# Kernel tuning notes

Measured on AMD Instinct MI355X. Metric: run time of the kernel, lower is better.

## Reference

```python
import jax, jax.numpy as jnp
import numpy as np

C = 128
NUM_GROUPS = 32  # min(32, 128 // 4)
EPS = 1e-6


def group_norm(x, gamma, beta):
    N, Cc, H, W = x.shape
    xg = x.reshape(N, NUM_GROUPS, -1)
    mean = xg.mean(axis=-1, keepdims=True)
    var = ((xg - mean) ** 2).mean(axis=-1, keepdims=True)
    xn = ((xg - mean) * jax.lax.rsqrt(var + EPS)).reshape(N, Cc, H, W)
    return xn * gamma[None, :, None, None] + beta[None, :, None, None]


def conv1x1(x, w, b):
    # w: [C_out, C_in], b: [C_out]; 1x1 conv == channel matmul
    return jnp.einsum('nchw,oc->nohw', x, w) + b[None, :, None, None]


def setup_inputs() -> dict:
    key = jax.random.key(0)
    ks = jax.random.split(key, 11)
    s = 1.0 / np.sqrt(C)
    return {
        'x': jax.random.normal(ks[0], (4, C, 64, 64), dtype=jnp.float32),
        'gamma': jnp.ones((C,), jnp.float32),
        'beta': jnp.zeros((C,), jnp.float32),
        'wq': jax.random.normal(ks[1], (C, C), jnp.float32) * s,
        'bq': jnp.zeros((C,), jnp.float32),
        'wk': jax.random.normal(ks[2], (C, C), jnp.float32) * s,
        'bk': jnp.zeros((C,), jnp.float32),
        'wv': jax.random.normal(ks[3], (C, C), jnp.float32) * s,
        'bv': jnp.zeros((C,), jnp.float32),
        'wo': jax.random.normal(ks[4], (C, C), jnp.float32) * s,
        'bo': jnp.zeros((C,), jnp.float32),
    }


def reference(x, gamma, beta, wq, bq, wk, bk, wv, bv, wo, bo):
    N, Cc, H, W = x.shape
    L = H * W
    xn = group_norm(x, gamma, beta)
    q = conv1x1(xn, wq, bq).reshape(N, Cc, L)  # [N,C,L]
    k = conv1x1(xn, wk, bk).reshape(N, Cc, L)
    v = conv1x1(xn, wv, bv).reshape(N, Cc, L)
    scale = 1.0 / jnp.sqrt(jnp.asarray(Cc, x.dtype))
    scores = jnp.einsum('ncl,ncm->nlm', q, k) * scale  # [N,L,L]
    weights = jax.nn.softmax(scores, axis=-1)
    attn = jnp.einsum('nlm,ncm->ncl', weights, v).reshape(N, Cc, H, W)
    return x + conv1x1(attn, wo, bo)
```

## Files before the change

kernel.cpp:

```cpp
#include <hip/hip_runtime.h>
#include <hip/hip_bf16.h>


#define N_B 4
#define C_D 128
#define L_D 4096
#define SPLIT 4
#define KVB 128
#define FSTEPS ((L_D/SPLIT)/KVB)
#define QSCALE (0.08838834764831845f * 1.4426950408889634f)
#define FIXM 16.0f

using f32x4  = __attribute__((ext_vector_type(4))) float;
using f32x16 = __attribute__((ext_vector_type(16))) float;
using bf16x8 = __attribute__((ext_vector_type(8))) short;

static __device__ __forceinline__ unsigned short f2bf(float f){
  return (unsigned short)((__builtin_bit_cast(unsigned int, f) + 0x8000u) >> 16);
}
static __device__ __forceinline__ float bf2f(unsigned short u){
  unsigned int x = ((unsigned int)u) << 16;
  return __builtin_bit_cast(float, x);
}
static __device__ __forceinline__ unsigned int pk2(float a, float b){
  unsigned int ua = __builtin_bit_cast(unsigned int, a) + 0x8000u;
  unsigned int ub = __builtin_bit_cast(unsigned int, b) + 0x8000u;
  return __builtin_amdgcn_perm(ub, ua, 0x07060302u);
}
static __device__ __forceinline__ float exp2a(float x){
  float r; asm("v_exp_f32 %0, %1" : "=v"(r) : "v"(x)); return r;
}
static __device__ __forceinline__ void gll16(const void* g, void* l){
  __builtin_amdgcn_global_load_lds(
      (const __attribute__((address_space(1))) unsigned int*)g,
      (__attribute__((address_space(3))) unsigned int*)l, 16, 0, 0);
}

__global__ __launch_bounds__(256) void gnw_k(
    const float* __restrict__ x, float* __restrict__ stats,
    const float* __restrict__ wq, const float* __restrict__ wk,
    const float* __restrict__ wv, const float* __restrict__ wo,
    unsigned short* __restrict__ wbf)
{
  int b = blockIdx.x, t = threadIdx.x;
  if (b >= 128){
    int b2 = b - 128;
    int mat = b2 >> 4;
    const float* src = (mat == 0) ? wq : (mat == 1) ? wk : (mat == 2) ? wv : wo;
    int off = (b2 & 15) * 1024 + t * 4;
    float4 v = *(const float4*)(src + off);
    *(uint2*)(wbf + mat*16384 + off) = make_uint2(pk2(v.x, v.y), pk2(v.z, v.w));
    return;
  }
  const float4* p = (const float4*)(x + (size_t)b * (4 * L_D));
  float s = 0.f, ss = 0.f;
#pragma unroll
  for (int i = 0; i < 16; ++i){
    float4 v = p[t + i*256];
    s  += v.x + v.y + v.z + v.w;
    ss += v.x*v.x + v.y*v.y + v.z*v.z + v.w*v.w;
  }
#pragma unroll
  for (int off = 32; off > 0; off >>= 1){
    s  += __shfl_down(s, off);
    ss += __shfl_down(ss, off);
  }
  __shared__ float rs4[4], rss4[4];
  if ((t & 63) == 0){ rs4[t>>6] = s; rss4[t>>6] = ss; }
  __syncthreads();
  if (t == 0){
    s  = rs4[0]+rs4[1]+rs4[2]+rs4[3];
    ss = rss4[0]+rss4[1]+rss4[2]+rss4[3];
    float mean = s * (1.f/16384.f);
    float var  = ss * (1.f/16384.f) - mean*mean;
    if (var < 0.f) var = 0.f;
    stats[2*b]   = mean;
    stats[2*b+1] = rsqrtf(var + 1e-6f);
  }
}

__global__ __launch_bounds__(256) void qkv_k(
    const float* __restrict__ x, const float* __restrict__ stats,
    const float* __restrict__ gamma, const float* __restrict__ beta,
    const unsigned short* __restrict__ wbf,
    const float* __restrict__ bq, const float* __restrict__ bk,
    const float* __restrict__ bv,
    unsigned short* __restrict__ q_ws, unsigned short* __restrict__ k_ws,
    unsigned short* __restrict__ v_ws)
{
  __shared__ unsigned short xnT[64][136];
  __shared__ unsigned short qbuf[64][136];

  int t = threadIdx.x, b = blockIdx.x;
  int wi = b >> 8;
  int bt = b & 255;
  int n = bt >> 6, l0 = (bt & 63) * 64;

  {
    int l = t & 63, cq = t >> 6;
#pragma unroll
    for (int it = 0; it < 8; ++it){
      int c0 = cq*4 + it*16;
      int g  = c0 >> 2;
      float mean = stats[(n*32+g)*2];
      float rstd = stats[(n*32+g)*2+1];
      float vv[4];
#pragma unroll
      for (int jj = 0; jj < 4; ++jj){
        int c = c0 + jj;
        float sc = rstd * gamma[c];
        float bs = beta[c] - mean * sc;
        vv[jj] = x[(size_t)(n*C_D + c)*L_D + l0 + l]*sc + bs;
      }
      *(unsigned int*)&xnT[l][c0]   = pk2(vv[0], vv[1]);
      *(unsigned int*)&xnT[l][c0+2] = pk2(vv[2], vv[3]);
    }
  }
  __syncthreads();

  int w = t >> 6, lane = t & 63, u = lane >> 4, l15 = lane & 15;
  int wc = w >> 1, wl = w & 1;
  const unsigned short* W = wbf + wi*16384;
  const float* Bv = (wi == 0) ? bq : (wi == 1) ? bk : bv;

  f32x4 zz = {0.f,0.f,0.f,0.f};
  f32x4 acc[4][2];
#pragma unroll
  for (int ct = 0; ct < 4; ++ct)
#pragma unroll
    for (int lt = 0; lt < 2; ++lt) acc[ct][lt] = zz;

#pragma unroll
  for (int kst = 0; kst < 4; ++kst){
    bf16x8 bfrag[2];
#pragma unroll
    for (int lt = 0; lt < 2; ++lt)
      bfrag[lt] = *(const bf16x8*)&xnT[32*wl + 16*lt + l15][kst*32 + 8*u];
#pragma unroll
    for (int ct = 0; ct < 4; ++ct){
      bf16x8 af = *(const bf16x8*)(W + (size_t)(64*wc + 16*ct + l15)*C_D + kst*32 + 8*u);
#pragma unroll
      for (int lt = 0; lt < 2; ++lt)
        acc[ct][lt] = __builtin_amdgcn_mfma_f32_16x16x32_bf16(af, bfrag[lt], acc[ct][lt], 0, 0, 0);
    }
  }

  if (wi < 2){
    float qs = (wi == 0) ? QSCALE : 1.0f;
#pragma unroll
    for (int ct = 0; ct < 4; ++ct){
      float bias[4];
#pragma unroll
      for (int r = 0; r < 4; ++r) bias[r] = Bv[64*wc + 16*ct + 4*u + r];
#pragma unroll
      for (int lt = 0; lt < 2; ++lt){
        float v0 = (acc[ct][lt][0] + bias[0]) * qs;
        float v1 = (acc[ct][lt][1] + bias[1]) * qs;
        float v2 = (acc[ct][lt][2] + bias[2]) * qs;
        float v3 = (acc[ct][lt][3] + bias[3]) * qs;
        int row = 32*wl + 16*lt + l15;
        int col = 64*wc + 16*ct + 4*u;
        *(unsigned int*)&qbuf[row][col]   = pk2(v0, v1);
        *(unsigned int*)&qbuf[row][col+2] = pk2(v2, v3);
      }
    }
    __syncthreads();
    {
      int l = t >> 2, ch = t & 3;
      unsigned short* dst = ((wi == 0) ? q_ws : k_ws) + (size_t)(n*L_D + l0 + l)*C_D + ch*32;
#pragma unroll
      for (int i = 0; i < 4; ++i)
        *(uint4*)(dst + i*8) = *(const uint4*)&qbuf[l][ch*32 + i*8];
    }
  } else {
    int p16 = (l15 & 3) | ((l15 & 4) << 1) | ((l15 & 8) >> 1);
#pragma unroll
    for (int ct = 0; ct < 4; ++ct){
      float bias[4];
#pragma unroll
      for (int r = 0; r < 4; ++r) bias[r] = Bv[64*wc + 16*ct + 4*u + r];
#pragma unroll
      for (int lt = 0; lt < 2; ++lt)
#pragma unroll
        for (int r = 0; r < 4; ++r){
          int co = 64*wc + 16*ct + 4*u + r;
          v_ws[(size_t)(n*C_D + co)*L_D + l0 + 32*wl + 16*lt + p16] =
              f2bf(acc[ct][lt][r] + bias[r]);
        }
    }
  }
}

__global__ __launch_bounds__(512, 2) void flash_split_k(
    const unsigned short* __restrict__ q_ws, const unsigned short* __restrict__ k_ws,
    const unsigned short* __restrict__ v_ws,
    unsigned short* __restrict__ po_ws, float* __restrict__ md_ws)
{
  __shared__ __align__(16) char shmem[131072];

  int t = threadIdx.x;
  int phys = blockIdx.x;
  int xcd = phys & 7, j = phys >> 3;
  int pair = xcd*8 + (j & 7);
  int s = j >> 3;
  int n = pair >> 4, lt256 = pair & 15;
  int l0 = lt256 * 256;
  int m_base = s * (L_D / SPLIT);
  int w = t >> 6, lane = t & 63, hi = lane >> 5, l31 = lane & 31;
  int lr = lane >> 4, ls = lane & 15;

  bf16x8 qf[8];
  {
    const unsigned short* qrow = q_ws + ((size_t)(n*L_D + l0 + 32*w + l31))*C_D;
#pragma unroll
    for (int kst = 0; kst < 8; ++kst)
      qf[kst] = *(const bf16x8*)(qrow + 16*kst + 8*hi);
  }

  f32x16 zz16;
#pragma unroll
  for (int i = 0; i < 16; ++i) zz16[i] = 0.f;
  f32x16 accO[4];
#pragma unroll
  for (int ct = 0; ct < 4; ++ct) accO[ct] = zz16;
  float rsum = 0.f;

  const unsigned short* kg[4];
  const unsigned short* vg[4];
  int ldof[4];
#pragma unroll
  for (int i = 0; i < 4; ++i){
    int row = 16*w + 4*i + lr;
    int ub = (ls << 4) ^ ((row & 15) << 4);
    kg[i] = k_ws + ((size_t)(n*L_D + m_base + row))*C_D + (ub >> 1);
    vg[i] = v_ws + ((size_t)(n*C_D + row))*L_D + m_base + (ub >> 1);
    ldof[i] = (16*w + 4*i)*256;
  }

  {
#pragma unroll
    for (int i = 0; i < 4; ++i){
      gll16(kg[i], shmem + ldof[i]);
      gll16(vg[i], shmem + 65536 + ldof[i]);
    }
  }
  __syncthreads();

#pragma unroll 2
  for (int step = 0; step < FSTEPS; ++step){
    int cur = step & 1, nxt = cur ^ 1;
    char* kB = shmem + (cur << 15);
    char* vB = shmem + 65536 + (cur << 15);

    if (step + 1 < FSTEPS){
      char* kN = shmem + (nxt << 15);
      char* vN = shmem + 65536 + (nxt << 15);
#pragma unroll
      for (int i = 0; i < 4; ++i){
        gll16(kg[i] + (size_t)(step+1)*KVB*C_D, kN + ldof[i]);
        gll16(vg[i] + (step+1)*KVB,             vN + ldof[i]);
      }
    }

    f32x16 accS[4];
#pragma unroll
    for (int mt = 0; mt < 4; ++mt) accS[mt] = zz16;
    __builtin_amdgcn_s_setprio(1);
#pragma unroll
    for (int mt = 0; mt < 4; ++mt){
      int row = 32*mt + l31;
      bf16x8 afr[8];
#pragma unroll
      for (int kst = 0; kst < 8; ++kst)
        afr[kst] = *(const bf16x8*)(kB + row*256 + ((32*kst + 16*hi) ^ ((row & 15) << 4)));
#pragma unroll
      for (int kst = 0; kst < 8; ++kst)
        accS[mt] = __builtin_amdgcn_mfma_f32_32x32x16_bf16(afr[kst], qf[kst], accS[mt], 0, 0, 0);
    }
    __builtin_amdgcn_s_setprio(0);

    union { unsigned int u[8]; bf16x8 h[2]; } Wm[4];
#pragma unroll
    for (int mt = 0; mt < 4; ++mt){
      float p[16];
#pragma unroll
      for (int r = 0; r < 16; ++r){ p[r] = exp2a(accS[mt][r] - FIXM); rsum += p[r]; }
#pragma unroll
      for (int wd = 0; wd < 8; ++wd) Wm[mt].u[wd] = pk2(p[2*wd], p[2*wd+1]);
    }

    __builtin_amdgcn_s_setprio(1);
#pragma unroll
    for (int sl = 0; sl < 8; ++sl){
      bf16x8 pf = Wm[sl >> 1].h[sl & 1];
      bf16x8 vfr[4];
#pragma unroll
      for (int ct = 0; ct < 4; ++ct){
        int vr = 32*ct + l31;
        vfr[ct] = *(const bf16x8*)(vB + vr*256 + ((32*sl + 16*hi) ^ ((vr & 15) << 4)));
      }
#pragma unroll
      for (int ct = 0; ct < 4; ++ct)
        accO[ct] = __builtin_amdgcn_mfma_f32_32x32x16_bf16(vfr[ct], pf, accO[ct], 0, 0, 0);
    }
    __builtin_amdgcn_s_setprio(0);
    __syncthreads();
  }

  rsum += __shfl_xor(rsum, 32);

  char* tB = shmem;
  {
    int lloc = 32*w + l31;
    int tsw = (lloc & 15) << 4;
    char* tr = tB + (size_t)lloc*256;
#pragma unroll
    for (int ct = 0; ct < 4; ++ct)
#pragma unroll
      for (int q = 0; q < 4; ++q){
        int cb2 = 64*ct + 16*q + 8*hi;
        *(unsigned int*)(tr + ((cb2    ) ^ tsw)) = pk2(accO[ct][4*q+0], accO[ct][4*q+1]);
        *(unsigned int*)(tr + ((cb2 + 4) ^ tsw)) = pk2(accO[ct][4*q+2], accO[ct][4*q+3]);
      }
  }
  __syncthreads();
  {
    int row2 = t >> 1, hf2 = t & 1;
    int tile = row2 >> 7, lrow = row2 & 127;
    size_t pb = ((size_t)((n*32 + 2*lt256 + tile)*SPLIT + s)) * (size_t)(128*128);
    unsigned short* dst = po_ws + pb + (size_t)lrow*128 + hf2*64;
    const char* srcr = tB + row2*256;
    int sw2 = (row2 & 15) << 4;
#pragma unroll
    for (int i = 0; i < 8; ++i)
      *(uint4*)(dst + 8*i) = *(const uint4*)(srcr + ((hf2*128 + 16*i) ^ sw2));
  }
  if (lane < 32){
    int lg = 32*w + lane;
    int tile2 = lg >> 7, lrow2 = lg & 127;
    size_t mb2 = ((size_t)((n*32 + 2*lt256 + tile2)*SPLIT + s)) * 128;
    md_ws[mb2 + lrow2] = rsum;
  }
}

__global__ __launch_bounds__(256) void combine_k(
    const unsigned short* __restrict__ po_ws, const float* __restrict__ md_ws,
    const float* __restrict__ x, const unsigned short* __restrict__ wo_bf,
    const float* __restrict__ bo, float* __restrict__ out)
{
  __shared__ __align__(16) char aB[16384];

  int t = threadIdx.x, b = blockIdx.x;
  int xcd = b & 7, j = b >> 3;
  int pair = xcd*8 + (j & 7);
  int quarter = j >> 3;
  int n = pair >> 4, lt256 = pair & 15;
  int lt64 = lt256*4 + quarter;
  int f = lt64 >> 1, loff = (lt64 & 1)*64, l0 = lt64*64;
  size_t pbase = ((size_t)((n*32 + f)*SPLIT)) * (size_t)(128*128);
  size_t mbase = ((size_t)((n*32 + f)*SPLIT)) * 128;

  {
    int l = t >> 2, q = t & 3;
    float Dg = 0.f;
#pragma unroll
    for (int s2 = 0; s2 < SPLIT; ++s2)
      Dg += md_ws[mbase + s2*128 + loff + l];
    float inv = 1.0f / Dg;

    float a[32];
#pragma unroll
    for (int i = 0; i < 32; ++i) a[i] = 0.f;
#pragma unroll
    for (int s2 = 0; s2 < SPLIT; ++s2){
      const uint4* p = (const uint4*)(po_ws + pbase + (size_t)s2*(128*128)
                                      + (size_t)(loff + l)*128 + q*32);
#pragma unroll
      for (int i = 0; i < 4; ++i){
        uint4 uv = p[i];
        unsigned int uu[4] = {uv.x, uv.y, uv.z, uv.w};
#pragma unroll
        for (int j2 = 0; j2 < 4; ++j2){
          a[8*i + 2*j2]     += bf2f((unsigned short)(uu[j2] & 0xffffu));
          a[8*i + 2*j2 + 1] += bf2f((unsigned short)(uu[j2] >> 16));
        }
      }
    }
    char* ar = aB + l*256;
    int asw = (l & 7) << 4;
#pragma unroll
    for (int i = 0; i < 16; ++i){
      int cb = q*64 + 4*i;
      *(unsigned int*)(ar + (cb ^ asw)) = pk2(a[2*i]*inv, a[2*i+1]*inv);
    }
  }
  __syncthreads();

  int w = t >> 6, lane = t & 63, hi = lane >> 5, l31 = lane & 31;
  int lh = w >> 1, ch = w & 1;
  f32x16 acc[2];
#pragma unroll
  for (int ci = 0; ci < 2; ++ci)
#pragma unroll
    for (int i = 0; i < 16; ++i) acc[ci][i] = 0.f;

#pragma unroll
  for (int kst = 0; kst < 8; ++kst){
    int row = 32*lh + l31;
    bf16x8 bfg = *(const bf16x8*)(aB + row*256 + ((32*kst + 16*hi) ^ ((row & 7) << 4)));
#pragma unroll
    for (int ci = 0; ci < 2; ++ci){
      bf16x8 af = *(const bf16x8*)(wo_bf + (size_t)(64*ch + 32*ci + l31)*C_D + 16*kst + 8*hi);
      acc[ci] = __builtin_amdgcn_mfma_f32_32x32x16_bf16(af, bfg, acc[ci], 0, 0, 0);
    }
  }
#pragma unroll
  for (int ci = 0; ci < 2; ++ci)
#pragma unroll
    for (int r = 0; r < 16; ++r){
      int o = 64*ch + 32*ci + (r & 3) + 8*(r >> 2) + 4*hi;
      size_t idx = (size_t)(n*C_D + o)*L_D + l0 + 32*lh + l31;
      out[idx] = x[idx] + bo[o] + acc[ci][r];
    }
}

extern "C" void kernel_launch(void* const* d_in, const int* in_sizes, int n_in,
                              void* d_out, int out_size, void* d_ws, size_t ws_size,
                              hipStream_t stream) {
  const float* x     = (const float*)d_in[0];
  const float* gamma = (const float*)d_in[1];
  const float* beta  = (const float*)d_in[2];
  const float* wq    = (const float*)d_in[3];
  const float* bq    = (const float*)d_in[4];
  const float* wk    = (const float*)d_in[5];
  const float* bk    = (const float*)d_in[6];
  const float* wv    = (const float*)d_in[7];
  const float* bv    = (const float*)d_in[8];
  const float* wo    = (const float*)d_in[9];
  const float* bo    = (const float*)d_in[10];
  float* out = (float*)d_out;

  char* ws = (char*)d_ws;
  float* stats          = (float*)ws;
  unsigned short* q_ws  = (unsigned short*)(ws + 4096);
  unsigned short* k_ws  = q_ws + (size_t)N_B * L_D * C_D;
  unsigned short* v_ws  = k_ws + (size_t)N_B * L_D * C_D;
  unsigned short* po_ws = v_ws + (size_t)N_B * L_D * C_D;
  float* md_ws          = (float*)(po_ws + (size_t)N_B * 32 * SPLIT * 128 * 128);
  unsigned short* wbf   = (unsigned short*)(md_ws + (size_t)N_B * 32 * SPLIT * 128);

  gnw_k<<<192, 256, 0, stream>>>(x, stats, wq, wk, wv, wo, wbf);
  qkv_k<<<768, 256, 0, stream>>>(x, stats, gamma, beta, wbf, bq, bk, bv,
                                 q_ws, k_ws, v_ws);
  flash_split_k<<<256, 512, 0, stream>>>(q_ws, k_ws, v_ws, po_ws, md_ws);
  combine_k<<<256, 256, 0, stream>>>(po_ws, md_ws, x, wbf + 3*16384, bo, out);
}
```

Baseline: 73.77 us.

## Fuse output projection into flash kernel, drop KV split, precompute normalized x

The flash attention kernel no longer splits the key/value range across blocks. Each block covers 64 query rows over the full sequence, and its 8 waves split the key tiles and reduce partial outputs through shared memory. The output projection and residual add now happen inside the flash kernel, which removes the combine kernel and the partial-output workspace traffic. The group-norm kernel writes normalized bf16 activations directly, and the QKV kernel loops over all three weight matrices per block. In exchange there are fewer blocks in flight, each block runs longer over the full sequence, and the cross-wave reduction adds shared-memory traffic.

```diff
diff --git a/kernel.cpp b/kernel.cpp
--- a/kernel.cpp
+++ b/kernel.cpp
@@ -5,9 +5,6 @@
 #define N_B 4
 #define C_D 128
 #define L_D 4096
-#define SPLIT 4
-#define KVB 128
-#define FSTEPS ((L_D/SPLIT)/KVB)
 #define QSCALE (0.08838834764831845f * 1.4426950408889634f)
 #define FIXM 16.0f
 
@@ -37,10 +34,11 @@
 }
 
 __global__ __launch_bounds__(256) void gnw_k(
-    const float* __restrict__ x, float* __restrict__ stats,
+    const float* __restrict__ x,
+    const float* __restrict__ gamma, const float* __restrict__ beta,
     const float* __restrict__ wq, const float* __restrict__ wk,
     const float* __restrict__ wv, const float* __restrict__ wo,
-    unsigned short* __restrict__ wbf)
+    unsigned short* __restrict__ wbf, unsigned short* __restrict__ xn)
 {
   int b = blockIdx.x, t = threadIdx.x;
   if (b >= 128){
@@ -53,10 +51,12 @@
     return;
   }
   const float4* p = (const float4*)(x + (size_t)b * (4 * L_D));
+  float4 vbuf[16];
   float s = 0.f, ss = 0.f;
 #pragma unroll
   for (int i = 0; i < 16; ++i){
     float4 v = p[t + i*256];
+    vbuf[i] = v;
     s  += v.x + v.y + v.z + v.w;
     ss += v.x*v.x + v.y*v.y + v.z*v.z + v.w*v.w;
   }
@@ -68,20 +68,35 @@
   __shared__ float rs4[4], rss4[4];
   if ((t & 63) == 0){ rs4[t>>6] = s; rss4[t>>6] = ss; }
   __syncthreads();
-  if (t == 0){
-    s  = rs4[0]+rs4[1]+rs4[2]+rs4[3];
-    ss = rss4[0]+rss4[1]+rss4[2]+rss4[3];
-    float mean = s * (1.f/16384.f);
-    float var  = ss * (1.f/16384.f) - mean*mean;
-    if (var < 0.f) var = 0.f;
-    stats[2*b]   = mean;
-    stats[2*b+1] = rsqrtf(var + 1e-6f);
+  s  = rs4[0]+rs4[1]+rs4[2]+rs4[3];
+  ss = rss4[0]+rss4[1]+rss4[2]+rss4[3];
+  float mean = s * (1.f/16384.f);
+  float var  = ss * (1.f/16384.f) - mean*mean;
+  if (var < 0.f) var = 0.f;
+  float rstd = rsqrtf(var + 1e-6f);
+
+  int cb = (b & 31) * 4;
+  float scv[4], bsv[4];
+#pragma unroll
+  for (int ch = 0; ch < 4; ++ch){
+    scv[ch] = rstd * gamma[cb + ch];
+    bsv[ch] = beta[cb + ch] - mean * scv[ch];
+  }
+  unsigned short* xo = xn + (size_t)b * (4 * L_D);
+#pragma unroll
+  for (int i = 0; i < 16; ++i){
+    int j  = t + i*256;
+    int ch = j >> 10;
+    float4 v = vbuf[i];
+    float sc = scv[ch], bs = bsv[ch];
+    float v0 = v.x*sc + bs, v1 = v.y*sc + bs;
+    float v2 = v.z*sc + bs, v3 = v.w*sc + bs;
+    *(uint2*)(xo + (size_t)j*4) = make_uint2(pk2(v0, v1), pk2(v2, v3));
   }
 }
 
 __global__ __launch_bounds__(256) void qkv_k(
-    const float* __restrict__ x, const float* __restrict__ stats,
-    const float* __restrict__ gamma, const float* __restrict__ beta,
+    const unsigned short* __restrict__ xn,
     const unsigned short* __restrict__ wbf,
     const float* __restrict__ bq, const float* __restrict__ bk,
     const float* __restrict__ bv,
@@ -92,126 +107,125 @@
   __shared__ unsigned short qbuf[64][136];
 
   int t = threadIdx.x, b = blockIdx.x;
-  int wi = b >> 8;
-  int bt = b & 255;
-  int n = bt >> 6, l0 = (bt & 63) * 64;
+  int n = b >> 6, l0 = (b & 63) * 64;
 
   {
     int l = t & 63, cq = t >> 6;
+    const unsigned short* xr = xn + ((size_t)n*C_D)*L_D + l0 + l;
 #pragma unroll
     for (int it = 0; it < 8; ++it){
       int c0 = cq*4 + it*16;
-      int g  = c0 >> 2;
-      float mean = stats[(n*32+g)*2];
-      float rstd = stats[(n*32+g)*2+1];
-      float vv[4];
-#pragma unroll
-      for (int jj = 0; jj < 4; ++jj){
-        int c = c0 + jj;
-        float sc = rstd * gamma[c];
-        float bs = beta[c] - mean * sc;
-        vv[jj] = x[(size_t)(n*C_D + c)*L_D + l0 + l]*sc + bs;
-      }
-      *(unsigned int*)&xnT[l][c0]   = pk2(vv[0], vv[1]);
-      *(unsigned int*)&xnT[l][c0+2] = pk2(vv[2], vv[3]);
+      unsigned int u0 = xr[(size_t)(c0+0)*L_D];
+      unsigned int u1 = xr[(size_t)(c0+1)*L_D];
+      unsigned int u2 = xr[(size_t)(c0+2)*L_D];
+      unsigned int u3 = xr[(size_t)(c0+3)*L_D];
+      *(unsigned int*)&xnT[l][c0]   = u0 | (u1 << 16);
+      *(unsigned int*)&xnT[l][c0+2] = u2 | (u3 << 16);
     }
   }
   __syncthreads();
 
   int w = t >> 6, lane = t & 63, u = lane >> 4, l15 = lane & 15;
   int wc = w >> 1, wl = w & 1;
-  const unsigned short* W = wbf + wi*16384;
-  const float* Bv = (wi == 0) ? bq : (wi == 1) ? bk : bv;
-
   f32x4 zz = {0.f,0.f,0.f,0.f};
-  f32x4 acc[4][2];
-#pragma unroll
-  for (int ct = 0; ct < 4; ++ct)
-#pragma unroll
-    for (int lt = 0; lt < 2; ++lt) acc[ct][lt] = zz;
-
-#pragma unroll
-  for (int kst = 0; kst < 4; ++kst){
-    bf16x8 bfrag[2];
-#pragma unroll
-    for (int lt = 0; lt < 2; ++lt)
-      bfrag[lt] = *(const bf16x8*)&xnT[32*wl + 16*lt + l15][kst*32 + 8*u];
-#pragma unroll
-    for (int ct = 0; ct < 4; ++ct){
-      bf16x8 af = *(const bf16x8*)(W + (size_t)(64*wc + 16*ct + l15)*C_D + kst*32 + 8*u);
+
+  for (int wi = 0; wi < 3; ++wi){
+    const unsigned short* W = wbf + wi*16384;
+    const float* Bv = (wi == 0) ? bq : (wi == 1) ? bk : bv;
+
+    f32x4 acc[4][2];
+#pragma unroll
+    for (int ct = 0; ct < 4; ++ct)
+#pragma unroll
+      for (int lt = 0; lt < 2; ++lt) acc[ct][lt] = zz;
+
+#pragma unroll
+    for (int kst = 0; kst < 4; ++kst){
+      bf16x8 bfrag[2];
 #pragma unroll
       for (int lt = 0; lt < 2; ++lt)
-        acc[ct][lt] = __builtin_amdgcn_mfma_f32_16x16x32_bf16(af, bfrag[lt], acc[ct][lt], 0, 0, 0);
-    }
-  }
-
-  if (wi < 2){
-    float qs = (wi == 0) ? QSCALE : 1.0f;
-#pragma unroll
-    for (int ct = 0; ct < 4; ++ct){
-      float bias[4];
-#pragma unroll
-      for (int r = 0; r < 4; ++r) bias[r] = Bv[64*wc + 16*ct + 4*u + r];
-#pragma unroll
-      for (int lt = 0; lt < 2; ++lt){
-        float v0 = (acc[ct][lt][0] + bias[0]) * qs;
-        float v1 = (acc[ct][lt][1] + bias[1]) * qs;
-        float v2 = (acc[ct][lt][2] + bias[2]) * qs;
-        float v3 = (acc[ct][lt][3] + bias[3]) * qs;
-        int row = 32*wl + 16*lt + l15;
-        int col = 64*wc + 16*ct + 4*u;
-        *(unsigned int*)&qbuf[row][col]   = pk2(v0, v1);
-        *(unsigned int*)&qbuf[row][col+2] = pk2(v2, v3);
-      }
-    }
-    __syncthreads();
-    {
-      int l = t >> 2, ch = t & 3;
-      unsigned short* dst = ((wi == 0) ? q_ws : k_ws) + (size_t)(n*L_D + l0 + l)*C_D + ch*32;
-#pragma unroll
-      for (int i = 0; i < 4; ++i)
-        *(uint4*)(dst + i*8) = *(const uint4*)&qbuf[l][ch*32 + i*8];
-    }
-  } else {
-    int p16 = (l15 & 3) | ((l15 & 4) << 1) | ((l15 & 8) >> 1);
-#pragma unroll
-    for (int ct = 0; ct < 4; ++ct){
-      float bias[4];
-#pragma unroll
-      for (int r = 0; r < 4; ++r) bias[r] = Bv[64*wc + 16*ct + 4*u + r];
-#pragma unroll
-      for (int lt = 0; lt < 2; ++lt)
-#pragma unroll
-        for (int r = 0; r < 4; ++r){
-          int co = 64*wc + 16*ct + 4*u + r;
-          v_ws[(size_t)(n*C_D + co)*L_D + l0 + 32*wl + 16*lt + p16] =
-              f2bf(acc[ct][lt][r] + bias[r]);
+        bfrag[lt] = *(const bf16x8*)&xnT[32*wl + 16*lt + l15][kst*32 + 8*u];
+#pragma unroll
+      for (int ct = 0; ct < 4; ++ct){
+        bf16x8 af = *(const bf16x8*)(W + (size_t)(64*wc + 16*ct + l15)*C_D + kst*32 + 8*u);
+#pragma unroll
+        for (int lt = 0; lt < 2; ++lt)
+          acc[ct][lt] = __builtin_amdgcn_mfma_f32_16x16x32_bf16(af, bfrag[lt], acc[ct][lt], 0, 0, 0);
+      }
+    }
+
+    if (wi < 2){
+      float qs = (wi == 0) ? QSCALE : 1.0f;
+      __syncthreads();
+#pragma unroll
+      for (int ct = 0; ct < 4; ++ct){
+        float bias[4];
+#pragma unroll
+        for (int r = 0; r < 4; ++r) bias[r] = Bv[64*wc + 16*ct + 4*u + r];
+#pragma unroll
+        for (int lt = 0; lt < 2; ++lt){
+          float v0 = (acc[ct][lt][0] + bias[0]) * qs;
+          float v1 = (acc[ct][lt][1] + bias[1]) * qs;
+          float v2 = (acc[ct][lt][2] + bias[2]) * qs;
+          float v3 = (acc[ct][lt][3] + bias[3]) * qs;
+          int row = 32*wl + 16*lt + l15;
+          int col = 64*wc + 16*ct + 4*u;
+          *(unsigned int*)&qbuf[row][col]   = pk2(v0, v1);
+          *(unsigned int*)&qbuf[row][col+2] = pk2(v2, v3);
         }
-    }
-  }
-}
-
-__global__ __launch_bounds__(512, 2) void flash_split_k(
+      }
+      __syncthreads();
+      {
+        int l = t >> 2, ch = t & 3;
+        unsigned short* dst = ((wi == 0) ? q_ws : k_ws) + (size_t)(n*L_D + l0 + l)*C_D + ch*32;
+#pragma unroll
+        for (int i = 0; i < 4; ++i)
+          *(uint4*)(dst + i*8) = *(const uint4*)&qbuf[l][ch*32 + i*8];
+      }
+    } else {
+      int p16 = (l15 & 3) | ((l15 & 4) << 1) | ((l15 & 8) >> 1);
+#pragma unroll
+      for (int ct = 0; ct < 4; ++ct){
+        float bias[4];
+#pragma unroll
+        for (int r = 0; r < 4; ++r) bias[r] = Bv[64*wc + 16*ct + 4*u + r];
+#pragma unroll
+        for (int lt = 0; lt < 2; ++lt)
+#pragma unroll
+          for (int r = 0; r < 4; ++r){
+            int co = 64*wc + 16*ct + 4*u + r;
+            v_ws[(size_t)(n*C_D + co)*L_D + l0 + 32*wl + 16*lt + p16] =
+                f2bf(acc[ct][lt][r] + bias[r]);
+          }
+      }
+    }
+  }
+}
+
+__global__ __launch_bounds__(512, 2) void flash_fused_k(
     const unsigned short* __restrict__ q_ws, const unsigned short* __restrict__ k_ws,
     const unsigned short* __restrict__ v_ws,
-    unsigned short* __restrict__ po_ws, float* __restrict__ md_ws)
+    const float* __restrict__ x, const unsigned short* __restrict__ wo_bf,
+    const float* __restrict__ bo, float* __restrict__ out)
 {
-  __shared__ __align__(16) char shmem[131072];
+  __shared__ __align__(64) char shmem[131072];
+  constexpr int MB = 128;
+  constexpr int STEPS = L_D / MB;
 
   int t = threadIdx.x;
   int phys = blockIdx.x;
-  int xcd = phys & 7, j = phys >> 3;
-  int pair = xcd*8 + (j & 7);
-  int s = j >> 3;
-  int n = pair >> 4, lt256 = pair & 15;
-  int l0 = lt256 * 256;
-  int m_base = s * (L_D / SPLIT);
+  int xcd = phys & 7;
+  int n = xcd >> 1;
+  int ltile = ((xcd & 1) << 5) + (phys >> 3);
+  int l0 = ltile * 64;
   int w = t >> 6, lane = t & 63, hi = lane >> 5, l31 = lane & 31;
   int lr = lane >> 4, ls = lane & 15;
+  int mt = w & 3, lh = w >> 2;
+  int swz = (l31 & 15) << 4;
 
   bf16x8 qf[8];
   {
-    const unsigned short* qrow = q_ws + ((size_t)(n*L_D + l0 + 32*w + l31))*C_D;
+    const unsigned short* qrow = q_ws + ((size_t)(n*L_D + l0 + 32*lh + l31))*C_D;
 #pragma unroll
     for (int kst = 0; kst < 8; ++kst)
       qf[kst] = *(const bf16x8*)(qrow + 16*kst + 8*hi);
@@ -232,196 +246,143 @@
   for (int i = 0; i < 4; ++i){
     int row = 16*w + 4*i + lr;
     int ub = (ls << 4) ^ ((row & 15) << 4);
-    kg[i] = k_ws + ((size_t)(n*L_D + m_base + row))*C_D + (ub >> 1);
-    vg[i] = v_ws + ((size_t)(n*C_D + row))*L_D + m_base + (ub >> 1);
+    kg[i] = k_ws + ((size_t)(n*L_D + row))*C_D + (ub >> 1);
+    vg[i] = v_ws + ((size_t)(n*C_D + row))*L_D + (ub >> 1);
     ldof[i] = (16*w + 4*i)*256;
   }
 
-  {
-#pragma unroll
-    for (int i = 0; i < 4; ++i){
-      gll16(kg[i], shmem + ldof[i]);
-      gll16(vg[i], shmem + 65536 + ldof[i]);
-    }
-  }
-  __syncthreads();
+#pragma unroll
+  for (int i = 0; i < 4; ++i) gll16(kg[i], shmem + ldof[i]);
+#pragma unroll
+  for (int i = 0; i < 4; ++i) gll16(vg[i], shmem + 65536 + ldof[i]);
+  asm volatile("s_waitcnt vmcnt(0)" ::: "memory");
+  __builtin_amdgcn_s_barrier();
+  asm volatile("" ::: "memory");
 
 #pragma unroll 2
-  for (int step = 0; step < FSTEPS; ++step){
-    int cur = step & 1, nxt = cur ^ 1;
+  for (int step = 0; step < STEPS; ++step){
+    int cur = step & 1;
+    if (step + 1 < STEPS){
+      char* kN = shmem + ((cur ^ 1) << 15);
+      char* vN = shmem + 65536 + ((cur ^ 1) << 15);
+#pragma unroll
+      for (int i = 0; i < 4; ++i)
+        gll16(kg[i] + (size_t)(step+1)*MB*C_D, kN + ldof[i]);
+#pragma unroll
+      for (int i = 0; i < 4; ++i)
+        gll16(vg[i] + (step+1)*MB, vN + ldof[i]);
+    }
     char* kB = shmem + (cur << 15);
     char* vB = shmem + 65536 + (cur << 15);
 
-    if (step + 1 < FSTEPS){
-      char* kN = shmem + (nxt << 15);
-      char* vN = shmem + 65536 + (nxt << 15);
-#pragma unroll
-      for (int i = 0; i < 4; ++i){
-        gll16(kg[i] + (size_t)(step+1)*KVB*C_D, kN + ldof[i]);
-        gll16(vg[i] + (step+1)*KVB,             vN + ldof[i]);
-      }
-    }
-
-    f32x16 accS[4];
-#pragma unroll
-    for (int mt = 0; mt < 4; ++mt) accS[mt] = zz16;
+    f32x16 accS = zz16;
+    {
+      int krow = 32*mt + l31;
+      bf16x8 afr[8];
+      __builtin_amdgcn_s_setprio(1);
+#pragma unroll
+      for (int k = 0; k < 8; ++k)
+        afr[k] = *(const bf16x8*)(kB + krow*256 + ((32*k + 16*hi) ^ swz));
+#pragma unroll
+      for (int k = 0; k < 8; ++k)
+        accS = __builtin_amdgcn_mfma_f32_32x32x16_bf16(afr[k], qf[k], accS, 0, 0, 0);
+      __builtin_amdgcn_s_setprio(0);
+    }
+
+    union { unsigned int u[8]; bf16x8 h[2]; } Wm;
+    {
+      float p[16];
+#pragma unroll
+      for (int r = 0; r < 16; ++r) p[r] = exp2a(accS[r] - FIXM);
+      float s0 = (p[0]+p[1])+(p[2]+p[3]),   s1 = (p[4]+p[5])+(p[6]+p[7]);
+      float s2 = (p[8]+p[9])+(p[10]+p[11]), s3 = (p[12]+p[13])+(p[14]+p[15]);
+      rsum += (s0+s1)+(s2+s3);
+#pragma unroll
+      for (int k = 0; k < 8; ++k) Wm.u[k] = pk2(p[2*k], p[2*k+1]);
+    }
+
     __builtin_amdgcn_s_setprio(1);
 #pragma unroll
-    for (int mt = 0; mt < 4; ++mt){
-      int row = 32*mt + l31;
-      bf16x8 afr[8];
-#pragma unroll
-      for (int kst = 0; kst < 8; ++kst)
-        afr[kst] = *(const bf16x8*)(kB + row*256 + ((32*kst + 16*hi) ^ ((row & 15) << 4)));
-#pragma unroll
-      for (int kst = 0; kst < 8; ++kst)
-        accS[mt] = __builtin_amdgcn_mfma_f32_32x32x16_bf16(afr[kst], qf[kst], accS[mt], 0, 0, 0);
-    }
-    __builtin_amdgcn_s_setprio(0);
-
-    union { unsigned int u[8]; bf16x8 h[2]; } Wm[4];
-#pragma unroll
-    for (int mt = 0; mt < 4; ++mt){
-      float p[16];
-#pragma unroll
-      for (int r = 0; r < 16; ++r){ p[r] = exp2a(accS[mt][r] - FIXM); rsum += p[r]; }
-#pragma unroll
-      for (int wd = 0; wd < 8; ++wd) Wm[mt].u[wd] = pk2(p[2*wd], p[2*wd+1]);
-    }
-
-    __builtin_amdgcn_s_setprio(1);
-#pragma unroll
-    for (int sl = 0; sl < 8; ++sl){
-      bf16x8 pf = Wm[sl >> 1].h[sl & 1];
+    for (int sl = 0; sl < 2; ++sl){
+      bf16x8 pf = Wm.h[sl];
       bf16x8 vfr[4];
 #pragma unroll
       for (int ct = 0; ct < 4; ++ct){
-        int vr = 32*ct + l31;
-        vfr[ct] = *(const bf16x8*)(vB + vr*256 + ((32*sl + 16*hi) ^ ((vr & 15) << 4)));
+        int c = 32*ct + l31;
+        vfr[ct] = *(const bf16x8*)(vB + c*256 + ((64*mt + 32*sl + 16*hi) ^ swz));
       }
 #pragma unroll
       for (int ct = 0; ct < 4; ++ct)
         accO[ct] = __builtin_amdgcn_mfma_f32_32x32x16_bf16(vfr[ct], pf, accO[ct], 0, 0, 0);
     }
     __builtin_amdgcn_s_setprio(0);
-    __syncthreads();
+
+    asm volatile("s_waitcnt vmcnt(0)" ::: "memory");
+    __builtin_amdgcn_s_barrier();
+    asm volatile("" ::: "memory");
   }
 
   rsum += __shfl_xor(rsum, 32);
 
-  char* tB = shmem;
+  if (lane < 32) *(float*)(shmem + w*128 + l31*4) = rsum;
+  __syncthreads();
+  float invD;
   {
-    int lloc = 32*w + l31;
+    const float* rs = (const float*)shmem;
+    int base = lh * 128;
+    float D = rs[base + l31] + rs[base + 32 + l31]
+            + rs[base + 64 + l31] + rs[base + 96 + l31];
+    invD = 1.0f / D;
+  }
+  if (mt != 0){
+    float* dst = (float*)(shmem + w*16384);
+#pragma unroll
+    for (int ct = 0; ct < 4; ++ct)
+      *(f32x16*)(dst + ct*1024 + lane*16) = accO[ct];
+  }
+  __syncthreads();
+  if (mt == 0){
+#pragma unroll
+    for (int m2 = 1; m2 < 4; ++m2){
+      const float* src = (const float*)(shmem + (w + m2)*16384);
+#pragma unroll
+      for (int ct = 0; ct < 4; ++ct)
+        accO[ct] += *(const f32x16*)(src + ct*1024 + lane*16);
+    }
+    int lloc = 32*lh + l31;
     int tsw = (lloc & 15) << 4;
-    char* tr = tB + (size_t)lloc*256;
+    char* tr = shmem + (size_t)lloc*256;
 #pragma unroll
     for (int ct = 0; ct < 4; ++ct)
 #pragma unroll
       for (int q = 0; q < 4; ++q){
         int cb2 = 64*ct + 16*q + 8*hi;
-        *(unsigned int*)(tr + ((cb2    ) ^ tsw)) = pk2(accO[ct][4*q+0], accO[ct][4*q+1]);
-        *(unsigned int*)(tr + ((cb2 + 4) ^ tsw)) = pk2(accO[ct][4*q+2], accO[ct][4*q+3]);
+        *(unsigned int*)(tr + ((cb2    ) ^ tsw)) = pk2(accO[ct][4*q+0]*invD, accO[ct][4*q+1]*invD);
+        *(unsigned int*)(tr + ((cb2 + 4) ^ tsw)) = pk2(accO[ct][4*q+2]*invD, accO[ct][4*q+3]*invD);
       }
   }
   __syncthreads();
+
   {
-    int row2 = t >> 1, hf2 = t & 1;
-    int tile = row2 >> 7, lrow = row2 & 127;
-    size_t pb = ((size_t)((n*32 + 2*lt256 + tile)*SPLIT + s)) * (size_t)(128*128);
-    unsigned short* dst = po_ws + pb + (size_t)lrow*128 + hf2*64;
-    const char* srcr = tB + row2*256;
-    int sw2 = (row2 & 15) << 4;
-#pragma unroll
-    for (int i = 0; i < 8; ++i)
-      *(uint4*)(dst + 8*i) = *(const uint4*)(srcr + ((hf2*128 + 16*i) ^ sw2));
-  }
-  if (lane < 32){
-    int lg = 32*w + lane;
-    int tile2 = lg >> 7, lrow2 = lg & 127;
-    size_t mb2 = ((size_t)((n*32 + 2*lt256 + tile2)*SPLIT + s)) * 128;
-    md_ws[mb2 + lrow2] = rsum;
-  }
-}
-
-__global__ __launch_bounds__(256) void combine_k(
-    const unsigned short* __restrict__ po_ws, const float* __restrict__ md_ws,
-    const float* __restrict__ x, const unsigned short* __restrict__ wo_bf,
-    const float* __restrict__ bo, float* __restrict__ out)
-{
-  __shared__ __align__(16) char aB[16384];
-
-  int t = threadIdx.x, b = blockIdx.x;
-  int xcd = b & 7, j = b >> 3;
-  int pair = xcd*8 + (j & 7);
-  int quarter = j >> 3;
-  int n = pair >> 4, lt256 = pair & 15;
-  int lt64 = lt256*4 + quarter;
-  int f = lt64 >> 1, loff = (lt64 & 1)*64, l0 = lt64*64;
-  size_t pbase = ((size_t)((n*32 + f)*SPLIT)) * (size_t)(128*128);
-  size_t mbase = ((size_t)((n*32 + f)*SPLIT)) * 128;
-
-  {
-    int l = t >> 2, q = t & 3;
-    float Dg = 0.f;
-#pragma unroll
-    for (int s2 = 0; s2 < SPLIT; ++s2)
-      Dg += md_ws[mbase + s2*128 + loff + l];
-    float inv = 1.0f / Dg;
-
-    float a[32];
-#pragma unroll
-    for (int i = 0; i < 32; ++i) a[i] = 0.f;
-#pragma unroll
-    for (int s2 = 0; s2 < SPLIT; ++s2){
-      const uint4* p = (const uint4*)(po_ws + pbase + (size_t)s2*(128*128)
-                                      + (size_t)(loff + l)*128 + q*32);
-#pragma unroll
-      for (int i = 0; i < 4; ++i){
-        uint4 uv = p[i];
-        unsigned int uu[4] = {uv.x, uv.y, uv.z, uv.w};
-#pragma unroll
-        for (int j2 = 0; j2 < 4; ++j2){
-          a[8*i + 2*j2]     += bf2f((unsigned short)(uu[j2] & 0xffffu));
-          a[8*i + 2*j2 + 1] += bf2f((unsigned short)(uu[j2] >> 16));
-        }
-      }
-    }
-    char* ar = aB + l*256;
-    int asw = (l & 7) << 4;
-#pragma unroll
-    for (int i = 0; i < 16; ++i){
-      int cb = q*64 + 4*i;
-      *(unsigned int*)(ar + (cb ^ asw)) = pk2(a[2*i]*inv, a[2*i+1]*inv);
-    }
-  }
-  __syncthreads();
-
-  int w = t >> 6, lane = t & 63, hi = lane >> 5, l31 = lane & 31;
-  int lh = w >> 1, ch = w & 1;
-  f32x16 acc[2];
-#pragma unroll
-  for (int ci = 0; ci < 2; ++ci)
-#pragma unroll
-    for (int i = 0; i < 16; ++i) acc[ci][i] = 0.f;
-
-#pragma unroll
-  for (int kst = 0; kst < 8; ++kst){
-    int row = 32*lh + l31;
-    bf16x8 bfg = *(const bf16x8*)(aB + row*256 + ((32*kst + 16*hi) ^ ((row & 7) << 4)));
-#pragma unroll
-    for (int ci = 0; ci < 2; ++ci){
-      bf16x8 af = *(const bf16x8*)(wo_bf + (size_t)(64*ch + 32*ci + l31)*C_D + 16*kst + 8*hi);
-      acc[ci] = __builtin_amdgcn_mfma_f32_32x32x16_bf16(af, bfg, acc[ci], 0, 0, 0);
-    }
-  }
-#pragma unroll
-  for (int ci = 0; ci < 2; ++ci)
+    int ow = w & 3, lh2 = w >> 2;
+    f32x16 acc;
+#pragma unroll
+    for (int i = 0; i < 16; ++i) acc[i] = 0.f;
+    int row = 32*lh2 + l31;
+    int bswz = (row & 15) << 4;
+#pragma unroll
+    for (int kst = 0; kst < 8; ++kst){
+      bf16x8 bfg = *(const bf16x8*)(shmem + row*256 + ((32*kst + 16*hi) ^ bswz));
+      bf16x8 af  = *(const bf16x8*)(wo_bf + (size_t)(32*ow + l31)*C_D + 16*kst + 8*hi);
+      acc = __builtin_amdgcn_mfma_f32_32x32x16_bf16(af, bfg, acc, 0, 0, 0);
+    }
 #pragma unroll
     for (int r = 0; r < 16; ++r){
-      int o = 64*ch + 32*ci + (r & 3) + 8*(r >> 2) + 4*hi;
-      size_t idx = (size_t)(n*C_D + o)*L_D + l0 + 32*lh + l31;
-      out[idx] = x[idx] + bo[o] + acc[ci][r];
-    }
+      int o = 32*ow + (r & 3) + 8*(r >> 2) + 4*hi;
+      size_t idx = (size_t)(n*C_D + o)*L_D + l0 + 32*lh2 + l31;
+      out[idx] = x[idx] + bo[o] + acc[r];
+    }
+  }
 }
 
 extern "C" void kernel_launch(void* const* d_in, const int* in_sizes, int n_in,
@@ -441,17 +402,14 @@
   float* out = (float*)d_out;
 
   char* ws = (char*)d_ws;
-  float* stats          = (float*)ws;
   unsigned short* q_ws  = (unsigned short*)(ws + 4096);
   unsigned short* k_ws  = q_ws + (size_t)N_B * L_D * C_D;
   unsigned short* v_ws  = k_ws + (size_t)N_B * L_D * C_D;
-  unsigned short* po_ws = v_ws + (size_t)N_B * L_D * C_D;
-  float* md_ws          = (float*)(po_ws + (size_t)N_B * 32 * SPLIT * 128 * 128);
-  unsigned short* wbf   = (unsigned short*)(md_ws + (size_t)N_B * 32 * SPLIT * 128);
-
-  gnw_k<<<192, 256, 0, stream>>>(x, stats, wq, wk, wv, wo, wbf);
-  qkv_k<<<768, 256, 0, stream>>>(x, stats, gamma, beta, wbf, bq, bk, bv,
-                                 q_ws, k_ws, v_ws);
-  flash_split_k<<<256, 512, 0, stream>>>(q_ws, k_ws, v_ws, po_ws, md_ws);
-  combine_k<<<256, 256, 0, stream>>>(po_ws, md_ws, x, wbf + 3*16384, bo, out);
-}
+  unsigned short* wbf   = v_ws + (size_t)N_B * L_D * C_D;
+  unsigned short* xn_ws = wbf + 4*16384;
+
+  gnw_k<<<192, 256, 0, stream>>>(x, gamma, beta, wq, wk, wv, wo, wbf, xn_ws);
+  qkv_k<<<256, 256, 0, stream>>>(xn_ws, wbf, bq, bk, bv, q_ws, k_ws, v_ws);
+  flash_fused_k<<<256, 512, 0, stream>>>(q_ws, k_ws, v_ws,
+                                         x, wbf + 3*16384, bo, out);
+}
```

Result: no change. 73.46 us (-0.4%).
